# Performance work log

Measured on AMD Instinct MI355X. Metric: run time of the kernel, lower is better.

Reference implementation:

```python
import math
import jax, jax.numpy as jnp
import numpy as np

B, N, C, H = 4, 2304, 512, 8  # batch, tokens (div by 3), channels, heads
HD = C // H


def setup_inputs() -> dict:
    key = jax.random.key(0)
    k0, k1, k2 = jax.random.split(key, 3)
    x = jax.random.normal(k0, (B, N, C), dtype=jnp.float32)
    # in_projection: Linear(C, 3C) with bias; out_projection: Linear(C, C)
    w_in = jax.random.normal(k1, (3 * C, C), dtype=jnp.float32) * 0.02
    b_in = jnp.zeros((3 * C,), dtype=jnp.float32)
    w_out = jax.random.normal(k2, (C, C), dtype=jnp.float32) * 0.02
    b_out = jnp.zeros((C,), dtype=jnp.float32)
    return {"x": x, "w_in": w_in, "b_in": b_in, "w_out": w_out, "b_out": b_out}


def reference(x, w_in, b_in, w_out, b_out):
    b, n, c = x.shape
    y = jnp.einsum('bnc,fc->bnf', x, w_in) + b_in            # [B, N, 3C]
    # Faithful to torch: chunk along the TOKEN axis (dim=1), then flat-reshape
    # each (B, N/3, 3C) chunk into (B, N, H, HD) -> transpose to (B, H, N, HD).
    def to_heads(t):
        return t.reshape(b, n, H, HD).transpose(0, 2, 1, 3)
    q, k, v = (to_heads(t) for t in jnp.split(y, 3, axis=1))
    # Unnormalized bilinear attention: NO softmax between the two matmuls.
    w = jnp.einsum('bhqd,bhkd->bhqk', q, k) / math.sqrt(HD)   # [B, H, N, N]
    o = jnp.einsum('bhqk,bhkd->bhqd', w, v)                   # [B, H, N, HD]
    o = o.transpose(0, 2, 1, 3).reshape(b, n, c)              # [B, N, C]
    return jnp.einsum('bnc,fc->bnf', o, w_out) + b_out
```

## Files before the change

kernel.cpp:

```cpp
#include <hip/hip_runtime.h>
#include <hip/hip_bf16.h>

#define BATCH 4
#define TOK   2304
#define CH    512
#define NHEAD 8
#define HDIM  64
#define F3    1536
#define YB_STRIDE ((long)TOK * F3)
#define QKV_SZ    ((long)TOK * CH)
#define KVCHUNK   9

typedef __attribute__((ext_vector_type(8))) short short8;
typedef __attribute__((ext_vector_type(4))) float f32x4;

__device__ inline ushort f2b(float f) {
    __hip_bfloat16 h = __float2bfloat16(f);
    return *reinterpret_cast<ushort*>(&h);
}
__device__ inline void unp(unsigned int u, float& lo, float& hi) {
    union { unsigned int i; float f; } a, c;
    a.i = u << 16; c.i = u & 0xffff0000u;
    lo = a.f; hi = c.f;
}

#define GLL(gp, lp) __builtin_amdgcn_global_load_lds( \
    (const __attribute__((address_space(1))) unsigned int*)(gp), \
    (__attribute__((address_space(3))) unsigned int*)(lp), 16, 0, 0)

__global__ __launch_bounds__(256) void cvt_bf16_2(
    const float* __restrict__ x, const float* __restrict__ w,
    ushort* __restrict__ xb_wb, int nx4, int nw4)
{
    const int i = blockIdx.x * 256 + threadIdx.x;
    float4 v;
    if (i < nx4)                v = ((const float4*)x)[i];
    else if (i < nx4 + nw4)     v = ((const float4*)w)[i - nx4];
    else return;
    ushort4 o;
    o.x = f2b(v.x); o.y = f2b(v.y); o.z = f2b(v.z); o.w = f2b(v.w);
    ((ushort4*)xb_wb)[i] = o;
}

template<int KDIM, bool OUT_BF16>
__global__ __launch_bounds__(512, 2) void gemm256_8ph(
    const ushort* __restrict__ A, const ushort* __restrict__ B,
    const float* __restrict__ bias, void* __restrict__ Cout, int N)
{
    constexpr int NT = KDIM / 64;
    __shared__ __align__(16) char smem[131072];

    const int tid  = threadIdx.x;
    const int lane = tid & 63, wave = tid >> 6;
    const int wm = wave >> 2, wn = wave & 3;

    const int nbx  = gridDim.x;
    const int flat = blockIdx.x + nbx * blockIdx.y;
    const int cpx  = (nbx * gridDim.y) >> 3;
    const int swz  = (flat & 7) * cpx + (flat >> 3);
    const int row0 = (swz / nbx) * 256, col0 = (swz % nbx) * 256;

    const int srow = tid >> 3;
    const int scol = ((tid & 7) ^ (srow & 7)) << 3;
    const ushort* gA = A + (long)(row0 + srow) * KDIM + scol;
    const ushort* gB = B + (long)(col0 + srow) * KDIM + scol;
    char* ldsW = smem + wave * 1024;

    const int l15 = lane & 15, lg = lane >> 4, l7 = lane & 7;
    const int cp[2] = { (lg * 16) ^ (l7 * 16), (64 + lg * 16) ^ (l7 * 16) };
    const char* rdA = smem + (wm * 128 + l15) * 128;
    const char* rdB = smem + 65536 + (wn * 64 + l15) * 128;

    f32x4  acc[8][4] = {};
    short8 a[2][4][2], b[2][2];

#define STAGE8(op, t, h) do { \
    const ushort* _g = ((op) ? gB : gA) + ((h) * 128) * KDIM + (t) * 64; \
    char* _l = ldsW + (op) * 65536 + ((t) & 1) * 32768 + (h) * 16384; \
    GLL(_g, _l); \
    GLL(_g + 64 * KDIM, _l + 8192); \
} while (0)

#define LDA8(t, mh) do { \
    const char* _p = rdA + ((t) & 1) * 32768 + (mh) * 8192; \
    _Pragma("unroll") for (int mf = 0; mf < 4; ++mf) { \
        a[mh][mf][0] = *(const short8*)(_p + mf * 2048 + cp[0]); \
        a[mh][mf][1] = *(const short8*)(_p + mf * 2048 + cp[1]); } \
} while (0)

#define LDB8(t, nh) do { \
    const char* _p = rdB + ((t) & 1) * 32768 + (nh) * 4096; \
    _Pragma("unroll") for (int j = 0; j < 2; ++j) { \
        b[j][0] = *(const short8*)(_p + j * 2048 + cp[0]); \
        b[j][1] = *(const short8*)(_p + j * 2048 + cp[1]); } \
} while (0)

#define MFMAQ(mh, nh) do { \
    _Pragma("unroll") for (int mf = 0; mf < 4; ++mf) \
    _Pragma("unroll") for (int j = 0; j < 2; ++j) \
    _Pragma("unroll") for (int ks = 0; ks < 2; ++ks) \
        acc[(mh)*4+mf][(nh)*2+j] = __builtin_amdgcn_mfma_f32_16x16x32_bf16( \
            a[mh][mf][ks], b[j][ks], acc[(mh)*4+mf][(nh)*2+j], 0, 0, 0); \
} while (0)

#define BAR8() __builtin_amdgcn_s_barrier()
#define VMC(n) asm volatile("s_waitcnt vmcnt(" #n ")" ::: "memory")

    STAGE8(0, 0, 0); STAGE8(0, 0, 1); STAGE8(1, 0, 0); STAGE8(1, 0, 1);
    VMC(4);
    STAGE8(1, 1, 0); STAGE8(0, 1, 0); STAGE8(0, 1, 1);
    VMC(6);
    BAR8();

#pragma unroll
    for (int t = 0; t < NT; ++t) {
        LDA8(t, 0); LDB8(t, 0);
        if (t + 1 < NT) STAGE8(1, t + 1, 1);
        BAR8(); __builtin_amdgcn_s_setprio(1); MFMAQ(0, 0); __builtin_amdgcn_s_setprio(0); BAR8();
        LDA8(t, 1);
        BAR8(); __builtin_amdgcn_s_setprio(1); MFMAQ(1, 0); __builtin_amdgcn_s_setprio(0); BAR8();
        LDB8(t, 1);
        if (t + 2 < NT) STAGE8(0, t + 2, 0);
        BAR8(); __builtin_amdgcn_s_setprio(1); MFMAQ(0, 1); __builtin_amdgcn_s_setprio(0); BAR8();
        if (t + 2 < NT) { STAGE8(0, t + 2, 1);
                          STAGE8(1, t + 2, 0); }
        BAR8(); __builtin_amdgcn_s_setprio(1); MFMAQ(1, 1); __builtin_amdgcn_s_setprio(0);
        if (t + 2 < NT)      { VMC(6); }
        else if (t + 1 < NT) { VMC(0); }
        if (t + 1 < NT) BAR8();
    }

    const int rb = row0 + wm * 128 + lg * 4;
    const int cb = col0 + wn * 64 + l15;
#pragma unroll
    for (int mf = 0; mf < 8; ++mf) {
#pragma unroll
        for (int nf = 0; nf < 4; ++nf) {
            const int c = cb + nf * 16;
            const float bv = bias[c];
            const long base = (long)(rb + mf * 16) * N + c;
#pragma unroll
            for (int r = 0; r < 4; ++r) {
                const float v = acc[mf][nf][r] + bv;
                if (OUT_BF16) ((ushort*)Cout)[base + (long)r * N] = f2b(v);
                else          ((float*)Cout)[base + (long)r * N]  = v;
            }
        }
    }
#undef STAGE8
#undef LDA8
#undef LDB8
#undef MFMAQ
#undef BAR8
#undef VMC
}

template<bool OUT_BF16>
__global__ __launch_bounds__(256) void mfma_gemm_nt(
    const ushort* __restrict__ A, const ushort* __restrict__ B,
    const float* __restrict__ bias, void* __restrict__ Cout,
    int M, int N, int K, long sA, long sB, long sC)
{
    const int gx = gridDim.x, gxy = gridDim.x * gridDim.y;
    const int flat = blockIdx.x + gx * blockIdx.y + gxy * blockIdx.z;
    const int cpx  = (gxy * gridDim.z) >> 3;
    const int swz  = (flat & 7) * cpx + (flat >> 3);
    const int bz = swz / gxy, rem = swz % gxy;
    const int row0 = (rem / gx) * 128, col0 = (rem % gx) * 128;

    A += (long)bz * sA;
    B += (long)bz * sB;

    __shared__ __align__(16) ushort As[128 * 32];
    __shared__ __align__(16) ushort Bs[128 * 32];

    const int tid  = threadIdx.x;
    const int lane = tid & 63;
    const int wave = tid >> 6;
    const int wr   = (wave >> 1) * 64;
    const int wc   = (wave & 1) * 64;

    const int sr = tid >> 2;
    const int sc = (tid & 3) * 8;
    const ushort* gA0 = A + (long)(row0 + sr) * K + sc;
    const ushort* gA1 = A + (long)(row0 + sr + 64) * K + sc;
    const ushort* gB0 = B + (long)(col0 + sr) * K + sc;
    const ushort* gB1 = B + (long)(col0 + sr + 64) * K + sc;

    char* lA = (char*)As + wave * 1024;
    char* lB = (char*)Bs + wave * 1024;

    const int fr = lane & 15;
    const int kg = (lane >> 4) * 8;

    f32x4 acc[4][4] = {};

    for (int k0 = 0; k0 < K; k0 += 32) {
        if (k0) __syncthreads();
        GLL(gA0 + k0, lA);
        GLL(gA1 + k0, lA + 4096);
        GLL(gB0 + k0, lB);
        GLL(gB1 + k0, lB + 4096);
        __syncthreads();

        short8 a[4], b[4];
        #pragma unroll
        for (int m = 0; m < 4; ++m)
            a[m] = *(const short8*)(As + (wr + m * 16 + fr) * 32 + kg);
        #pragma unroll
        for (int n = 0; n < 4; ++n)
            b[n] = *(const short8*)(Bs + (wc + n * 16 + fr) * 32 + kg);

        #pragma unroll
        for (int m = 0; m < 4; ++m)
            #pragma unroll
            for (int n = 0; n < 4; ++n)
                acc[m][n] = __builtin_amdgcn_mfma_f32_16x16x32_bf16(
                    a[m], b[n], acc[m][n], 0, 0, 0);
    }

    const int rbase = row0 + wr + (lane >> 4) * 4;
    const int cbase = col0 + wc + (lane & 15);
    const long zoff = (long)bz * sC;
    #pragma unroll
    for (int m = 0; m < 4; ++m) {
        #pragma unroll
        for (int n = 0; n < 4; ++n) {
            const int c = cbase + n * 16;
            const float bv = bias[c];
            #pragma unroll
            for (int r = 0; r < 4; ++r) {
                const long off = zoff + (long)(rbase + m * 16 + r) * N + c;
                const float v = acc[m][n][r] + bv;
                if (OUT_BF16) ((ushort*)Cout)[off] = f2b(v);
                else          ((float*)Cout)[off]  = v;
            }
        }
    }
}

__global__ __launch_bounds__(256) void ktv_partial(
    const ushort* __restrict__ y, ushort* __restrict__ Mtp)
{
    const int chunk = blockIdx.x;
    const int bh    = blockIdx.y;
    const int b = bh >> 3, h = bh & 7;
    const ushort* Kp = y + (long)b * YB_STRIDE + QKV_SZ     + h * HDIM;
    const ushort* Vp = y + (long)b * YB_STRIDE + 2 * QKV_SZ + h * HDIM;

    __shared__ __align__(16) float Ks[64][68];
    __shared__ __align__(16) float Vs[64][68];

    const int tid = threadIdx.x;
    const int tx = tid & 15, ty = tid >> 4;
    const int lr = tid >> 2;
    const int ls = (tid & 3) * 16;

    float acc[4][4] = {};

    for (int s = 0; s < 4; ++s) {
        const int n0 = chunk * 256 + s * 64;
        const ushort* kr = Kp + (long)(n0 + lr) * CH + ls;
        const ushort* vr = Vp + (long)(n0 + lr) * CH + ls;
        const uint4 k0 = *(const uint4*)kr;
        const uint4 k1 = *(const uint4*)(kr + 8);
        const uint4 v0 = *(const uint4*)vr;
        const uint4 v1 = *(const uint4*)(vr + 8);
        if (s) __syncthreads();
        unsigned int kw[8] = {k0.x,k0.y,k0.z,k0.w,k1.x,k1.y,k1.z,k1.w};
        unsigned int vw[8] = {v0.x,v0.y,v0.z,v0.w,v1.x,v1.y,v1.z,v1.w};
        #pragma unroll
        for (int u = 0; u < 4; ++u) {
            float4 kf, vf;
            unp(kw[2*u],   kf.x, kf.y); unp(kw[2*u+1], kf.z, kf.w);
            unp(vw[2*u],   vf.x, vf.y); unp(vw[2*u+1], vf.z, vf.w);
            *(float4*)&Ks[lr][ls + 4*u] = kf;
            *(float4*)&Vs[lr][ls + 4*u] = vf;
        }
        __syncthreads();

        #pragma unroll 8
        for (int nn = 0; nn < 64; ++nn) {
            const float4 ka = *(const float4*)&Ks[nn][ty * 4];
            const float4 vb = *(const float4*)&Vs[nn][tx * 4];
            const float kk[4] = {ka.x, ka.y, ka.z, ka.w};
            const float vv[4] = {vb.x, vb.y, vb.z, vb.w};
            #pragma unroll
            for (int i = 0; i < 4; ++i)
                #pragma unroll
                for (int j = 0; j < 4; ++j)
                    acc[i][j] = fmaf(kk[i], vv[j], acc[i][j]);
        }
        __syncthreads();
    }

    ushort* Mo = Mtp + ((long)chunk * 32 + bh) * 4096;
    #pragma unroll
    for (int j = 0; j < 4; ++j) {
        ushort4 st;
        st.x = f2b(acc[0][j] * 0.125f); st.y = f2b(acc[1][j] * 0.125f);
        st.z = f2b(acc[2][j] * 0.125f); st.w = f2b(acc[3][j] * 0.125f);
        *(ushort4*)&Mo[(tx * 4 + j) * 64 + ty * 4] = st;
    }
}

__global__ __launch_bounds__(256) void fold_pt(
    const ushort* __restrict__ Mtp, const float* __restrict__ w_out,
    ushort* __restrict__ Pt)
{
    const int fc = blockIdx.x;
    const int bh = blockIdx.y;
    const int b = bh >> 3, h = bh & 7;

    __shared__ __align__(16) float Ms[64][68];
    __shared__ __align__(16) float Ws[64][68];

    const int tid = threadIdx.x;
    const int tx = tid & 15, ty = tid >> 4;
    const int r  = tid >> 2, c0 = (tid & 3) * 16;

    {
        const float* wr_ = w_out + (long)(fc * 64 + r) * CH + h * HDIM + c0;
        #pragma unroll
        for (int k = 0; k < 4; ++k)
            *(float4*)&Ws[r][c0 + 4 * k] = *(const float4*)(wr_ + 4 * k);
    }

    {
        const int e0 = tid * 16;
        float s[16] = {};
        #pragma unroll
        for (int c = 0; c < KVCHUNK; ++c) {
            const ushort* p = Mtp + ((long)c * 32 + bh) * 4096 + e0;
            const uint4 u0 = *(const uint4*)p;
            const uint4 u1 = *(const uint4*)(p + 8);
            const unsigned int uu[8] = {u0.x,u0.y,u0.z,u0.w,u1.x,u1.y,u1.z,u1.w};
            #pragma unroll
            for (int k = 0; k < 8; ++k) {
                float lo, hi; unp(uu[k], lo, hi);
                s[2*k] += lo; s[2*k+1] += hi;
            }
        }
        #pragma unroll
        for (int k = 0; k < 4; ++k) {
            float4 v; v.x = s[4*k]; v.y = s[4*k+1]; v.z = s[4*k+2]; v.w = s[4*k+3];
            *(float4*)&Ms[r][c0 + 4 * k] = v;
        }
    }
    __syncthreads();

    float acc[4][4] = {};
    for (int d = 0; d < 64; ++d) {
        const float4 mv = *(const float4*)&Ms[d][tx * 4];
        const float mm[4] = {mv.x, mv.y, mv.z, mv.w};
        #pragma unroll
        for (int i = 0; i < 4; ++i) {
            const float w = Ws[ty * 4 + i][d];
            #pragma unroll
            for (int j = 0; j < 4; ++j)
                acc[i][j] = fmaf(w, mm[j], acc[i][j]);
        }
    }
    const int fbase = fc * 64 + ty * 4;
    #pragma unroll
    for (int i = 0; i < 4; ++i) {
        ushort4 o;
        o.x = f2b(acc[i][0]); o.y = f2b(acc[i][1]);
        o.z = f2b(acc[i][2]); o.w = f2b(acc[i][3]);
        *(ushort4*)&Pt[(((long)b * CH) + fbase + i) * CH + h * HDIM + tx * 4] = o;
    }
}

extern "C" void kernel_launch(void* const* d_in, const int* in_sizes, int n_in,
                              void* d_out, int out_size, void* d_ws, size_t ws_size,
                              hipStream_t stream)
{
    const float* x     = (const float*)d_in[0];
    const float* w_in  = (const float*)d_in[1];
    const float* b_in  = (const float*)d_in[2];
    const float* w_out = (const float*)d_in[3];
    const float* b_out = (const float*)d_in[4];
    float* out = (float*)d_out;

    char* ws = (char*)d_ws;
    ushort* xb   = (ushort*)ws;
    ushort* wb   = (ushort*)(ws + 9437184);
    ushort* y    = (ushort*)(ws + 11010048);
    ushort* Mtp  = (ushort*)(ws + 39321600);
    ushort* Pt   = (ushort*)(ws + 41680896);

    cvt_bf16_2<<<5376, 256, 0, stream>>>(x, w_in, xb, 1179648, 196608);

    gemm256_8ph<512, true><<<dim3(F3 / 256, (BATCH * TOK) / 256), 512, 0, stream>>>(
        xb, wb, b_in, y, F3);

    ktv_partial<<<dim3(KVCHUNK, BATCH * NHEAD), 256, 0, stream>>>(y, Mtp);

    fold_pt<<<dim3(8, BATCH * NHEAD), 256, 0, stream>>>(Mtp, w_out, Pt);

    mfma_gemm_nt<false><<<dim3(CH / 128, TOK / 128, BATCH), 256, 0, stream>>>(
        y, Pt, b_out, out, TOK, CH, CH, YB_STRIDE, (long)CH * CH, QKV_SZ);
}
```

Measured before the change: 71.30 us.

## Compute K^T V partials with bf16 MFMA and fewer larger token chunks

Replaces the scalar fp32 FMA K^T·V partial kernel with a bf16 MFMA version. K and V tiles are stored transposed in LDS with an XOR swizzle to limit bank conflicts. The token chunk size grows from 256 to 384, cutting the partial count from 9 to 6 per head, and the workspace offset is updated to match. The aim is to cut ALU time in this stage, at the cost of fewer blocks (192 instead of 288) and scattered 2-byte LDS writes during the transpose.

```diff
diff --git a/kernel.cpp b/kernel.cpp
--- a/kernel.cpp
+++ b/kernel.cpp
@@ -9,7 +9,7 @@
 #define F3    1536
 #define YB_STRIDE ((long)TOK * F3)
 #define QKV_SZ    ((long)TOK * CH)
-#define KVCHUNK   9
+#define KVCHUNK   6
 
 typedef __attribute__((ext_vector_type(8))) short short8;
 typedef __attribute__((ext_vector_type(4))) float f32x4;
@@ -239,7 +239,7 @@
     }
 }
 
-__global__ __launch_bounds__(256) void ktv_partial(
+__global__ __launch_bounds__(256) void ktv_mfma(
     const ushort* __restrict__ y, ushort* __restrict__ Mtp)
 {
     const int chunk = blockIdx.x;
@@ -248,59 +248,68 @@
     const ushort* Kp = y + (long)b * YB_STRIDE + QKV_SZ     + h * HDIM;
     const ushort* Vp = y + (long)b * YB_STRIDE + 2 * QKV_SZ + h * HDIM;
 
-    __shared__ __align__(16) float Ks[64][68];
-    __shared__ __align__(16) float Vs[64][68];
-
-    const int tid = threadIdx.x;
-    const int tx = tid & 15, ty = tid >> 4;
-    const int lr = tid >> 2;
-    const int ls = (tid & 3) * 16;
-
-    float acc[4][4] = {};
-
-    for (int s = 0; s < 4; ++s) {
-        const int n0 = chunk * 256 + s * 64;
-        const ushort* kr = Kp + (long)(n0 + lr) * CH + ls;
-        const ushort* vr = Vp + (long)(n0 + lr) * CH + ls;
+    __shared__ __align__(16) ushort Kt[64 * 64];
+    __shared__ __align__(16) ushort Vt[64 * 64];
+
+    const int tid  = threadIdx.x;
+    const int lane = tid & 63, w = tid >> 6;
+    const int tloc = tid >> 2;
+    const int d0   = (tid & 3) * 16;
+
+    const int fr = lane & 15;
+    const int kg = (lane >> 4) * 8;
+    const int swr = (fr & 7) << 3;
+
+    f32x4 acc[4] = {};
+
+    for (int s = 0; s < 6; ++s) {
+        const int n0 = chunk * 384 + s * 64;
+        const ushort* kr = Kp + (long)(n0 + tloc) * CH + d0;
+        const ushort* vr = Vp + (long)(n0 + tloc) * CH + d0;
         const uint4 k0 = *(const uint4*)kr;
         const uint4 k1 = *(const uint4*)(kr + 8);
         const uint4 v0 = *(const uint4*)vr;
         const uint4 v1 = *(const uint4*)(vr + 8);
         if (s) __syncthreads();
-        unsigned int kw[8] = {k0.x,k0.y,k0.z,k0.w,k1.x,k1.y,k1.z,k1.w};
-        unsigned int vw[8] = {v0.x,v0.y,v0.z,v0.w,v1.x,v1.y,v1.z,v1.w};
-        #pragma unroll
-        for (int u = 0; u < 4; ++u) {
-            float4 kf, vf;
-            unp(kw[2*u],   kf.x, kf.y); unp(kw[2*u+1], kf.z, kf.w);
-            unp(vw[2*u],   vf.x, vf.y); unp(vw[2*u+1], vf.z, vf.w);
-            *(float4*)&Ks[lr][ls + 4*u] = kf;
-            *(float4*)&Vs[lr][ls + 4*u] = vf;
+        const unsigned int kw[8] = {k0.x,k0.y,k0.z,k0.w,k1.x,k1.y,k1.z,k1.w};
+        const unsigned int vw[8] = {v0.x,v0.y,v0.z,v0.w,v1.x,v1.y,v1.z,v1.w};
+        #pragma unroll
+        for (int j = 0; j < 16; ++j) {
+            const int d   = d0 + j;
+            const int idx = d * 64 + (tloc ^ ((d & 7) << 3));
+            const ushort kv = (ushort)(kw[j >> 1] >> ((j & 1) * 16));
+            const ushort vv = (ushort)(vw[j >> 1] >> ((j & 1) * 16));
+            Kt[idx] = kv;
+            Vt[idx] = vv;
         }
         __syncthreads();
 
-        #pragma unroll 8
-        for (int nn = 0; nn < 64; ++nn) {
-            const float4 ka = *(const float4*)&Ks[nn][ty * 4];
-            const float4 vb = *(const float4*)&Vs[nn][tx * 4];
-            const float kk[4] = {ka.x, ka.y, ka.z, ka.w};
-            const float vv[4] = {vb.x, vb.y, vb.z, vb.w};
-            #pragma unroll
-            for (int i = 0; i < 4; ++i)
-                #pragma unroll
-                for (int j = 0; j < 4; ++j)
-                    acc[i][j] = fmaf(kk[i], vv[j], acc[i][j]);
-        }
-        __syncthreads();
+        short8 a[4][2], bfrag[2];
+        #pragma unroll
+        for (int ks = 0; ks < 2; ++ks) {
+            const int kc = (kg + 32 * ks) ^ swr;
+            bfrag[ks] = *(const short8*)(Vt + (16 * w + fr) * 64 + kc);
+            #pragma unroll
+            for (int m = 0; m < 4; ++m)
+                a[m][ks] = *(const short8*)(Kt + (16 * m + fr) * 64 + kc);
+        }
+        #pragma unroll
+        for (int ks = 0; ks < 2; ++ks)
+            #pragma unroll
+            for (int m = 0; m < 4; ++m)
+                acc[m] = __builtin_amdgcn_mfma_f32_16x16x32_bf16(
+                    a[m][ks], bfrag[ks], acc[m], 0, 0, 0);
     }
 
     ushort* Mo = Mtp + ((long)chunk * 32 + bh) * 4096;
+    const int e  = 16 * w + fr;
+    const int lg = lane >> 4;
     #pragma unroll
-    for (int j = 0; j < 4; ++j) {
+    for (int m = 0; m < 4; ++m) {
         ushort4 st;
-        st.x = f2b(acc[0][j] * 0.125f); st.y = f2b(acc[1][j] * 0.125f);
-        st.z = f2b(acc[2][j] * 0.125f); st.w = f2b(acc[3][j] * 0.125f);
-        *(ushort4*)&Mo[(tx * 4 + j) * 64 + ty * 4] = st;
+        st.x = f2b(acc[m][0] * 0.125f); st.y = f2b(acc[m][1] * 0.125f);
+        st.z = f2b(acc[m][2] * 0.125f); st.w = f2b(acc[m][3] * 0.125f);
+        *(ushort4*)&Mo[e * 64 + 16 * m + lg * 4] = st;
     }
 }
 
@@ -387,14 +396,14 @@
     ushort* wb   = (ushort*)(ws + 9437184);
     ushort* y    = (ushort*)(ws + 11010048);
     ushort* Mtp  = (ushort*)(ws + 39321600);
-    ushort* Pt   = (ushort*)(ws + 41680896);
+    ushort* Pt   = (ushort*)(ws + 40894464);
 
     cvt_bf16_2<<<5376, 256, 0, stream>>>(x, w_in, xb, 1179648, 196608);
 
     gemm256_8ph<512, true><<<dim3(F3 / 256, (BATCH * TOK) / 256), 512, 0, stream>>>(
         xb, wb, b_in, y, F3);
 
-    ktv_partial<<<dim3(KVCHUNK, BATCH * NHEAD), 256, 0, stream>>>(y, Mtp);
+    ktv_mfma<<<dim3(KVCHUNK, BATCH * NHEAD), 256, 0, stream>>>(y, Mtp);
 
     fold_pt<<<dim3(8, BATCH * NHEAD), 256, 0, stream>>>(Mtp, w_out, Pt);
 
```

Result: faster. 60.17 us (-15.6%).
